# Optimization experiments

Hardware: AMD Instinct MI355X
Metric: run time of the kernel (lower is better)

The kernel has to match this reference:

```python
import jax, jax.numpy as jnp
import numpy as np

EPS = 1e-9       # module's displacement/convergence epsilon
COS_EPS = 1e-8   # torch F.cosine_similarity eps (norms clamped at eps)
LN_EPS = 1e-5


def _safe_norm(sq):
    # sqrt with zero-safe gradient for exactly-zero (padded) vectors
    return jnp.where(sq > 0, jnp.sqrt(jnp.maximum(sq, 1e-30)), 0.0)


def _features(coords, n):
    """coords: [S, md] padded; n: true length (>=4). Returns [60] features."""
    S, md = coords.shape
    f32 = coords.dtype
    nf = n.astype(f32)
    idx_d = jnp.arange(S - 1)
    m = n - 1                       # number of valid deltas
    mf = m.astype(f32)
    dmask = idx_d < m
    dmaskf = dmask.astype(f32)

    deltas = (coords[1:] - coords[:-1]) * dmaskf[:, None]     # [S-1, md]
    dmags = _safe_norm(jnp.sum(deltas * deltas, axis=-1))      # [S-1]

    last = jnp.take(coords, n - 1, axis=0)
    total_disp = _safe_norm(jnp.sum((last - coords[0]) ** 2))
    path_len = jnp.sum(dmags)
    disp_ratio = total_disp / (path_len + EPS)
    n_steps_norm = nf / 10.0

    # consecutive cosine similarities / curvatures (valid count = n-2)
    na = jnp.maximum(dmags, COS_EPS)
    cos = jnp.sum(deltas[:-1] * deltas[1:], axis=-1) / (na[:-1] * na[1:])  # [S-2]
    idx_c = jnp.arange(S - 2)
    cmask = idx_c < (n - 2)
    cmaskf = cmask.astype(f32)
    ncf = (n - 2).astype(f32)
    curv = 1.0 - cos
    curv_m = jnp.where(cmask, curv, 0.0)
    mean_curv = jnp.sum(curv_m) / ncf
    max_curv = jnp.max(jnp.where(cmask, curv, -jnp.inf))
    min_curv = jnp.min(jnp.where(cmask, curv, jnp.inf))
    curv_var = jnp.sum(cmaskf * (curv - mean_curv) ** 2) / jnp.maximum(ncf - 1.0, 1.0)
    std_curv = jnp.where(ncf > 1.0, jnp.sqrt(jnp.maximum(curv_var, 1e-30)), 0.0)
    curv_range = max_curv - min_curv

    mean_cos = jnp.sum(jnp.where(cmask, cos, 0.0)) / ncf
    min_cos = jnp.min(jnp.where(cmask, cos, jnp.inf))
    dir_changes = jnp.sum(cmaskf * (cos < 0).astype(f32)) / jnp.maximum(ncf, 1.0)

    linearity = disp_ratio
    loop_score = 1.0 - total_disp / (path_len + EPS)

    half = m // 2
    fmaskf = (idx_d < half + 1).astype(f32)
    smaskf = ((idx_d >= half) & (idx_d < m)).astype(f32)
    first_half = jnp.sum(dmags * fmaskf) / (half + 1).astype(f32)
    second_half = jnp.sum(dmags * smaskf) / (m - half).astype(f32)
    convergence = (first_half - second_half) / (first_half + EPS)
    cascade = (second_half - first_half) / (first_half + EPS)

    # all-pairs cosine (the O(n^2) block) via one GEMM per sample
    cosmat = (deltas @ deltas.T) / (na[:, None] * na[None, :])  # [S-1, S-1]
    pmask = (idx_d[:, None] < idx_d[None, :]) & (idx_d[None, :] < m)
    npairs = mf * (mf - 1.0) / 2.0
    parallelism = jnp.sum(jnp.where(pmask, cosmat, 0.0)) / jnp.maximum(npairs, 1.0)

    mean_dm = path_len / mf
    dm_var = jnp.sum(dmaskf * (dmags - mean_dm) ** 2) / jnp.maximum(mf - 1.0, 1.0)
    std_dm = jnp.where(mf > 1.0, jnp.sqrt(jnp.maximum(dm_var, 1e-30)), 0.0)
    max_dm = jnp.max(jnp.where(dmask, dmags, -jnp.inf))
    jump = jnp.where(mean_dm > EPS, max_dm / mean_dm, 1.0)

    rmaskf = (jnp.arange(S) < n).astype(f32)
    cnt = nf * md
    mean_coord = jnp.sum(coords * rmaskf[:, None]) / cnt
    coord_var = jnp.sum(rmaskf[:, None] * (coords - mean_coord) ** 2) / (cnt - 1.0)
    std_coord = jnp.sqrt(jnp.maximum(coord_var, 1e-30))

    scalars = jnp.stack([
        total_disp, path_len, disp_ratio, n_steps_norm,
        mean_curv, max_curv, std_curv, curv_range,
        mean_cos, min_cos, dir_changes,
        linearity, loop_score, convergence, parallelism, jump, cascade,
        mean_dm, std_dm, mean_coord, std_coord,
    ])  # [21]
    padded_deltas = deltas[:3].reshape(-1)   # [30] (masked -> already zero-padded)
    padded_curvs = curv_m[:9]                # [9]
    return jnp.concatenate([scalars, padded_deltas, padded_curvs])  # [60]


def setup_inputs() -> dict:
    key = jax.random.key(0)
    ks = jax.random.split(key, 4)
    B, S, md, H = 32768, 48, 10, 48
    coords = jax.random.normal(ks[0], (B, S, md), dtype=jnp.float32)
    lengths = jax.random.randint(ks[1], (B,), 4, S + 1, dtype=jnp.int32)
    W = jax.random.normal(ks[2], (60, H), dtype=jnp.float32) * 0.1
    b = jax.random.normal(ks[3], (H,), dtype=jnp.float32) * 0.01
    ln_w = jnp.ones((H,), dtype=jnp.float32)
    ln_b = jnp.zeros((H,), dtype=jnp.float32)
    return {"coords": coords, "lengths": lengths, "W": W, "b": b, "ln_w": ln_w, "ln_b": ln_b}


def reference(coords, lengths, W, b, ln_w, ln_b):
    feats = jax.vmap(_features)(coords, lengths)          # [B, 60]
    h = feats @ W + b                                     # [B, 48]
    mu = jnp.mean(h, axis=-1, keepdims=True)
    var = jnp.mean((h - mu) ** 2, axis=-1, keepdims=True)
    h = (h - mu) / jnp.sqrt(var + LN_EPS) * ln_w + ln_b
    return jax.nn.gelu(h, approximate=False)              # dropout is identity at eval
```

## Files before the change

### kernel.cpp

```cpp
#include <hip/hip_runtime.h>
#include <math.h>

static __device__ __forceinline__ float frcp(float x){ return __builtin_amdgcn_rcpf(x); }
static __device__ __forceinline__ float fsq (float x){ return __builtin_amdgcn_sqrtf(x); }

template<int CTRL>
static __device__ __forceinline__ float dppadd(float x){
  int t = __builtin_amdgcn_update_dpp(0, __float_as_int(x), CTRL, 0xf, 0xf, true);
  return x + __int_as_float(t);
}
template<int CTRL>
static __device__ __forceinline__ float dppmax(float x){
  int t = __builtin_amdgcn_update_dpp(__float_as_int(x), __float_as_int(x), CTRL, 0xf, 0xf, false);
  return fmaxf(x, __int_as_float(t));
}
template<int CTRL>
static __device__ __forceinline__ float dppmin(float x){
  int t = __builtin_amdgcn_update_dpp(__float_as_int(x), __float_as_int(x), CTRL, 0xf, 0xf, false);
  return fminf(x, __int_as_float(t));
}
static __device__ __forceinline__ float rsum16(float x){
  x = dppadd<0x111>(x); x = dppadd<0x112>(x);
  x = dppadd<0x114>(x); x = dppadd<0x118>(x);
  return __int_as_float(__builtin_amdgcn_ds_swizzle(__float_as_int(x), 0x1F0));
}
static __device__ __forceinline__ float rmax16(float x){
  x = dppmax<0x111>(x); x = dppmax<0x112>(x);
  x = dppmax<0x114>(x); x = dppmax<0x118>(x);
  return __int_as_float(__builtin_amdgcn_ds_swizzle(__float_as_int(x), 0x1F0));
}
static __device__ __forceinline__ float rmin16(float x){
  x = dppmin<0x111>(x); x = dppmin<0x112>(x);
  x = dppmin<0x114>(x); x = dppmin<0x118>(x);
  return __int_as_float(__builtin_amdgcn_ds_swizzle(__float_as_int(x), 0x1F0));
}
#define BC(P, x) __int_as_float(__builtin_amdgcn_ds_swizzle(__float_as_int(x), 0x10 | ((P) << 5)))

__global__ void transpose_w(const float* __restrict__ W, float* __restrict__ Wt){
  int idx = blockIdx.x * 256 + threadIdx.x;
  if (idx < 60 * 48) { int f = idx / 48, j = idx - f * 48; Wt[j * 60 + f] = W[idx]; }
}

template<bool USEWT>
__global__ __launch_bounds__(256)
void traj_kernel(const float* __restrict__ coords,
                 const int* __restrict__ lengths,
                 const float* __restrict__ Wsrc,
                 const float* __restrict__ bias,
                 const float* __restrict__ lnw,
                 const float* __restrict__ lnb,
                 float* __restrict__ out, int B)
{
  const int lane = threadIdx.x & 63;
  const int s    = lane & 15;
  const int grp  = (blockIdx.x * 4 + (threadIdx.x >> 6)) * 4 + (lane >> 4);
  const bool bvalid = (grp < B);
  const int b = bvalid ? grp : (B - 1);

  const int n = lengths[b];
  const int m = n - 1;
  const float* cp = coords + (size_t)b * 480;

  float c[3][10], cn[3][10];
#pragma unroll
  for (int q = 0; q < 3; ++q) {
    const float2* p = reinterpret_cast<const float2*>(cp + (q * 16 + s) * 10);
#pragma unroll
    for (int k = 0; k < 5; ++k) { float2 v = p[k]; c[q][2*k] = v.x; c[q][2*k+1] = v.y; }
  }
#pragma unroll
  for (int q = 0; q < 3; ++q) {
    const int row = q * 16 + s + 1;
    if (row < 48) {
      const float2* p = reinterpret_cast<const float2*>(cp + row * 10);
#pragma unroll
      for (int k = 0; k < 5; ++k) { float2 v = p[k]; cn[q][2*k] = v.x; cn[q][2*k+1] = v.y; }
    } else {
#pragma unroll
      for (int k = 0; k < 10; ++k) cn[q][k] = 0.f;
    }
  }

  float csl = 0.f, cs2l = 0.f;
#pragma unroll
  for (int q = 0; q < 3; ++q) {
    float t1 = 0.f, t2 = 0.f;
#pragma unroll
    for (int k = 0; k < 10; ++k) { t1 += c[q][k]; t2 = fmaf(c[q][k], c[q][k], t2); }
    const bool act = (q * 16 + s) < n;
    csl  += act ? t1 : 0.f;
    cs2l += act ? t2 : 0.f;
  }
  const float sum_c  = rsum16(csl);
  const float sum_c2 = rsum16(cs2l);

  float cc0[10];
#pragma unroll
  for (int k = 0; k < 10; ++k) cc0[k] = BC(0, c[0][k]);
  const int qs = (n - 1) >> 4, ssl = (n - 1) & 15;
  float tql = 0.f;
#pragma unroll
  for (int q = 0; q < 3; ++q) {
    float tq = 0.f;
#pragma unroll
    for (int k = 0; k < 10; ++k) { float t = c[q][k] - cc0[k]; tq = fmaf(t, t, tq); }
    tql = (s == ssl && q == qs) ? tq : tql;
  }
  const float tdq = rsum16(tql);
  const float total_disp = (tdq > 0.f) ? fsq(fmaxf(tdq, 1e-30f)) : 0.f;

  const int half = m >> 1;
  float d[3][10], inv[3];
  float path_l=0.f, dm2_l=0.f, maxdm_l=0.f, sf_l=0.f, ss_l=0.f, uu_l=0.f;
  float uk[10];
#pragma unroll
  for (int k = 0; k < 10; ++k) uk[k] = 0.f;
#pragma unroll
  for (int q = 0; q < 3; ++q) {
    const int j = q * 16 + s;
    float ds_ = 0.f;
#pragma unroll
    for (int k = 0; k < 10; ++k) { float dd = cn[q][k] - c[q][k]; d[q][k] = dd; ds_ = fmaf(dd, dd, ds_); }
    const float sn = (ds_ > 0.f) ? fsq(fmaxf(ds_, 1e-30f)) : 0.f;
    inv[q] = frcp(fmaxf(sn, 1e-8f));
    const bool jm = j < m;
    const float dm = jm ? sn : 0.f;
    path_l += dm;
    dm2_l  += jm ? ds_ : 0.f;
    maxdm_l = fmaxf(maxdm_l, dm);
    sf_l += (j <= half) ? dm : 0.f;
    ss_l += (j >= half) ? dm : 0.f;
    const float invm = jm ? inv[q] : 0.f;
#pragma unroll
    for (int k = 0; k < 10; ++k) uk[k] = fmaf(d[q][k], invm, uk[k]);
    uu_l = fmaf(ds_ * invm, invm, uu_l);
  }

  const int rotb = (((lane & 48) | ((lane + 1) & 15)) << 2);
  const float rinv0 = __int_as_float(__builtin_amdgcn_ds_bpermute(rotb, __float_as_int(inv[0])));
  const float rinv1 = __int_as_float(__builtin_amdgcn_ds_bpermute(rotb, __float_as_int(inv[1])));
  const float rinv2 = __int_as_float(__builtin_amdgcn_ds_bpermute(rotb, __float_as_int(inv[2])));
  float invn[3];
  invn[0] = (s < 15) ? rinv0 : rinv1;
  invn[1] = (s < 15) ? rinv1 : rinv2;
  invn[2] = (s < 15) ? rinv2 : 0.f;

  float cos_l=0.f, cos2_l=0.f, ng_l=0.f, maxc_l=-INFINITY, minc_l=INFINITY;
  float curv0 = 0.f;
#pragma unroll
  for (int q = 0; q < 3; ++q) {
    const int j = q * 16 + s;
    float dn[10];
    if (j + 2 < 48) {
      const float2* p = reinterpret_cast<const float2*>(cp + (j + 2) * 10);
#pragma unroll
      for (int k = 0; k < 5; ++k) { float2 v = p[k]; dn[2*k] = v.x - cn[q][2*k]; dn[2*k+1] = v.y - cn[q][2*k+1]; }
    } else {
#pragma unroll
      for (int k = 0; k < 10; ++k) dn[k] = 0.f;
    }
    float dot = 0.f;
#pragma unroll
    for (int k = 0; k < 10; ++k) dot = fmaf(d[q][k], dn[k], dot);
    const float cosv = dot * inv[q] * invn[q];
    const bool ca = j < (n - 2);
    const float cm = ca ? cosv : 0.f;
    cos_l += cm;
    cos2_l = fmaf(cm, cm, cos2_l);
    maxc_l = fmaxf(maxc_l, ca ? cosv : -INFINITY);
    minc_l = fminf(minc_l, ca ? cosv :  INFINITY);
    ng_l += (cm < 0.f) ? 1.f : 0.f;
    if (q == 0) curv0 = ca ? (1.f - cosv) : 0.f;
  }

  const float path_len = rsum16(path_l);
  const float sum_dm2  = rsum16(dm2_l);
  const float max_dm   = rmax16(maxdm_l);
  const float sum_f    = rsum16(sf_l);
  const float sum_s    = rsum16(ss_l);
  const float sum_cos  = rsum16(cos_l);
  const float sum_cos2 = rsum16(cos2_l);
  const float sum_ng   = rsum16(ng_l);
  const float max_cos  = rmax16(maxc_l);
  const float min_cos  = rmin16(minc_l);
  float Usq = 0.f;
#pragma unroll
  for (int k = 0; k < 10; ++k) { float Uk = rsum16(uk[k]); Usq = fmaf(Uk, Uk, Usq); }
  const float sum_uu = rsum16(uu_l);

  const float EPSf = 1e-9f;
  const float nf = (float)n, mf = (float)m, ncf = (float)(n - 2);
  const float rncf = frcp(ncf);
  const float disp_ratio = total_disp * frcp(path_len + EPSf);
  const float sum_cv  = ncf - sum_cos;
  const float mean_cv = sum_cv * rncf;
  const float sum_cv2 = fmaf(-2.f, sum_cos, ncf) + sum_cos2;
  const float cv_var  = (sum_cv2 - ncf * mean_cv * mean_cv) * frcp(fmaxf(ncf - 1.f, 1.f));
  const float std_cv  = fsq(fmaxf(cv_var, 1e-30f));
  const float max_cv  = 1.f - min_cos;
  const float cv_rng  = max_cos - min_cos;
  const float mean_cs = sum_cos * rncf;
  const float dirchg  = sum_ng * rncf;
  const float fh = sum_f * frcp((float)(half + 1));
  const float sh = sum_s * frcp((float)(m - half));
  const float conv = (fh - sh) * frcp(fh + EPSf);
  const float npairs = mf * (mf - 1.f) * 0.5f;
  const float par = (Usq - sum_uu) * 0.5f * frcp(npairs);
  const float mean_dm = path_len * frcp(mf);
  const float dm_var = (sum_dm2 - mf * mean_dm * mean_dm) * frcp(mf - 1.f);
  const float std_dm = fsq(fmaxf(dm_var, 1e-30f));
  const float jump = (mean_dm > EPSf) ? max_dm * frcp(mean_dm) : 1.f;
  const float cnt = nf * 10.f;
  const float mean_co = sum_c * frcp(cnt);
  const float co_var = (sum_c2 - cnt * mean_co * mean_co) * frcp(cnt - 1.f);
  const float std_co = fsq(fmaxf(co_var, 1e-30f));

  float feat[60];
  feat[0]  = total_disp;
  feat[1]  = path_len;
  feat[2]  = disp_ratio;
  feat[3]  = nf * 0.1f;
  feat[4]  = mean_cv;
  feat[5]  = max_cv;
  feat[6]  = std_cv;
  feat[7]  = cv_rng;
  feat[8]  = mean_cs;
  feat[9]  = min_cos;
  feat[10] = dirchg;
  feat[11] = disp_ratio;
  feat[12] = 1.f - disp_ratio;
  feat[13] = conv;
  feat[14] = par;
  feat[15] = jump;
  feat[16] = -conv;
  feat[17] = mean_dm;
  feat[18] = std_dm;
  feat[19] = mean_co;
  feat[20] = std_co;
#pragma unroll
  for (int k = 0; k < 10; ++k) feat[21 + k] = BC(0, d[0][k]);
#pragma unroll
  for (int k = 0; k < 10; ++k) feat[31 + k] = BC(1, d[0][k]);
#pragma unroll
  for (int k = 0; k < 10; ++k) feat[41 + k] = BC(2, d[0][k]);
  feat[51] = BC(0, curv0); feat[52] = BC(1, curv0); feat[53] = BC(2, curv0);
  feat[54] = BC(3, curv0); feat[55] = BC(4, curv0); feat[56] = BC(5, curv0);
  feat[57] = BC(6, curv0); feat[58] = BC(7, curv0); feat[59] = BC(8, curv0);

  float h[3];
#pragma unroll
  for (int q = 0; q < 3; ++q) {
    const int j = q * 16 + s;
    float acc = bias[j];
    if (USEWT) {
      const float4* wr = reinterpret_cast<const float4*>(Wsrc + j * 60);
#pragma unroll
      for (int t = 0; t < 15; ++t) {
        float4 w = wr[t];
        acc = fmaf(feat[4*t+0], w.x, acc);
        acc = fmaf(feat[4*t+1], w.y, acc);
        acc = fmaf(feat[4*t+2], w.z, acc);
        acc = fmaf(feat[4*t+3], w.w, acc);
      }
    } else {
#pragma unroll
      for (int f = 0; f < 60; ++f) acc = fmaf(feat[f], Wsrc[f * 48 + j], acc);
    }
    h[q] = acc;
  }

  const float s1 = rsum16(h[0] + h[1] + h[2]);
  const float s2 = rsum16(fmaf(h[0], h[0], fmaf(h[1], h[1], h[2] * h[2])));
  const float mu  = s1 * (1.f / 48.f);
  const float var = fmaf(-mu, mu, s2 * (1.f / 48.f));
  const float rstd = __builtin_amdgcn_rsqf(var + 1e-5f);

  if (bvalid) {
#pragma unroll
    for (int q = 0; q < 3; ++q) {
      const int j = q * 16 + s;
      float x = (h[q] - mu) * rstd * lnw[j] + lnb[j];
      float x2 = x * x;
      float u  = 0.7978845608f * x * fmaf(0.044715f, x2, 1.f);
      float e  = __builtin_amdgcn_exp2f(u * 2.885390082f);
      float th = fmaf(-2.f, frcp(1.f + e), 1.f);
      out[(size_t)b * 48 + j] = 0.5f * x * (1.f + th);
    }
  }
}

extern "C" void kernel_launch(void* const* d_in, const int* in_sizes, int n_in,
                              void* d_out, int out_size, void* d_ws, size_t ws_size,
                              hipStream_t stream)
{
  const float* coords = (const float*)d_in[0];
  const int*   lengths= (const int*)d_in[1];
  const float* W      = (const float*)d_in[2];
  const float* bias   = (const float*)d_in[3];
  const float* lnw    = (const float*)d_in[4];
  const float* lnb    = (const float*)d_in[5];
  float* out = (float*)d_out;

  const int B = in_sizes[1];
  const int blocks = (B + 15) / 16;

  if (ws_size >= (size_t)(60 * 48 * sizeof(float))) {
    float* Wt = (float*)d_ws;
    transpose_w<<<12, 256, 0, stream>>>(W, Wt);
    traj_kernel<true><<<blocks, 256, 0, stream>>>(coords, lengths, Wt, bias, lnw, lnb, out, B);
  } else {
    traj_kernel<false><<<blocks, 256, 0, stream>>>(coords, lengths, W, bias, lnw, lnb, out, B);
  }
}
```

Before: 122.3 us.

## Stage block's coordinates in LDS with coalesced float4 loads; split matvec accumulators

Each block of 16 trajectories now copies its whole contiguous coordinate slab (16x480 floats) into shared memory with coalesced float4 loads before any compute. All later strided row reads (current, next and next-next rows) come from LDS instead of global memory. This is meant to cut poorly coalesced, redundant global traffic, at the cost of 30KB of LDS per block, which may limit occupancy, plus a block barrier. Separately, the feature-by-weight dot product uses two independent accumulators to shorten the FMA dependency chain.

```diff
diff --git a/kernel.cpp b/kernel.cpp
--- a/kernel.cpp
+++ b/kernel.cpp
@@ -51,20 +51,39 @@
                  const float* __restrict__ lnb,
                  float* __restrict__ out, int B)
 {
-  const int lane = threadIdx.x & 63;
+  __shared__ float lds_c[16 * 480];
+
+  const int tid  = threadIdx.x;
+  const int lane = tid & 63;
   const int s    = lane & 15;
-  const int grp  = (blockIdx.x * 4 + (threadIdx.x >> 6)) * 4 + (lane >> 4);
+  const int T    = ((tid >> 6) << 2) | (lane >> 4);
+  const int blk  = blockIdx.x;
+  const int grp  = blk * 16 + T;
   const bool bvalid = (grp < B);
   const int b = bvalid ? grp : (B - 1);
 
+  {
+    const int lastblk = (B - 1) >> 4;
+    const int sblk = (blk <= lastblk) ? blk : lastblk;
+    const float4* g = reinterpret_cast<const float4*>(coords + (size_t)sblk * 7680);
+    float4* l = reinterpret_cast<float4*>(lds_c);
+    const int nvec = min(1920, (B - sblk * 16) * 120);
+#pragma unroll
+    for (int it = 0; it < 8; ++it) {
+      int idx = tid + it * 256;
+      if (idx < nvec) l[idx] = g[idx];
+    }
+  }
+  __syncthreads();
+
   const int n = lengths[b];
   const int m = n - 1;
-  const float* cp = coords + (size_t)b * 480;
+  const float* myc = lds_c + T * 480;
 
   float c[3][10], cn[3][10];
 #pragma unroll
   for (int q = 0; q < 3; ++q) {
-    const float2* p = reinterpret_cast<const float2*>(cp + (q * 16 + s) * 10);
+    const float2* p = reinterpret_cast<const float2*>(myc + (q * 16 + s) * 10);
 #pragma unroll
     for (int k = 0; k < 5; ++k) { float2 v = p[k]; c[q][2*k] = v.x; c[q][2*k+1] = v.y; }
   }
@@ -72,7 +91,7 @@
   for (int q = 0; q < 3; ++q) {
     const int row = q * 16 + s + 1;
     if (row < 48) {
-      const float2* p = reinterpret_cast<const float2*>(cp + row * 10);
+      const float2* p = reinterpret_cast<const float2*>(myc + row * 10);
 #pragma unroll
       for (int k = 0; k < 5; ++k) { float2 v = p[k]; cn[q][2*k] = v.x; cn[q][2*k+1] = v.y; }
     } else {
@@ -152,7 +171,7 @@
     const int j = q * 16 + s;
     float dn[10];
     if (j + 2 < 48) {
-      const float2* p = reinterpret_cast<const float2*>(cp + (j + 2) * 10);
+      const float2* p = reinterpret_cast<const float2*>(myc + (j + 2) * 10);
 #pragma unroll
       for (int k = 0; k < 5; ++k) { float2 v = p[k]; dn[2*k] = v.x - cn[q][2*k]; dn[2*k+1] = v.y - cn[q][2*k+1]; }
     } else {
@@ -251,22 +270,32 @@
 #pragma unroll
   for (int q = 0; q < 3; ++q) {
     const int j = q * 16 + s;
-    float acc = bias[j];
+    float acc0 = bias[j], acc1 = 0.f;
     if (USEWT) {
       const float4* wr = reinterpret_cast<const float4*>(Wsrc + j * 60);
 #pragma unroll
-      for (int t = 0; t < 15; ++t) {
+      for (int t = 0; t < 15; t += 2) {
         float4 w = wr[t];
-        acc = fmaf(feat[4*t+0], w.x, acc);
-        acc = fmaf(feat[4*t+1], w.y, acc);
-        acc = fmaf(feat[4*t+2], w.z, acc);
-        acc = fmaf(feat[4*t+3], w.w, acc);
+        acc0 = fmaf(feat[4*t+0], w.x, acc0);
+        acc0 = fmaf(feat[4*t+1], w.y, acc0);
+        acc0 = fmaf(feat[4*t+2], w.z, acc0);
+        acc0 = fmaf(feat[4*t+3], w.w, acc0);
+        if (t + 1 < 15) {
+          float4 w1 = wr[t+1];
+          acc1 = fmaf(feat[4*t+4], w1.x, acc1);
+          acc1 = fmaf(feat[4*t+5], w1.y, acc1);
+          acc1 = fmaf(feat[4*t+6], w1.z, acc1);
+          acc1 = fmaf(feat[4*t+7], w1.w, acc1);
+        }
       }
     } else {
 #pragma unroll
-      for (int f = 0; f < 60; ++f) acc = fmaf(feat[f], Wsrc[f * 48 + j], acc);
-    }
-    h[q] = acc;
+      for (int f = 0; f < 60; f += 2) {
+        acc0 = fmaf(feat[f],   Wsrc[f * 48 + j], acc0);
+        acc1 = fmaf(feat[f+1], Wsrc[(f+1) * 48 + j], acc1);
+      }
+    }
+    h[q] = acc0 + acc1;
   }
 
   const float s1 = rsum16(h[0] + h[1] + h[2]);
```

After: 125.6 us. +2.7%, slower.

## Stage W and features in LDS, reduce scalars in one lane

Applied to the files above, without the earlier changes.

The projection weights are now staged once per block in shared memory, and the 60 per-trajectory features are written to a per-group LDS buffer instead of being broadcast into every lane's registers. Reductions skip the final swizzle broadcast: lane 15, which holds the full 16-lane sum, computes all scalar features alone and stores them. Total displacement is computed directly from rows 0 and n-1 in that same lane. The aim is to cut register pressure (launch bounds now ask for 4 blocks per SM), swizzle traffic and redundant global W loads, at the cost of a block sync, LDS reads and serial scalar work in one lane.

```diff
diff --git a/kernel.cpp b/kernel.cpp
--- a/kernel.cpp
+++ b/kernel.cpp
@@ -19,30 +19,35 @@
   int t = __builtin_amdgcn_update_dpp(__float_as_int(x), __float_as_int(x), CTRL, 0xf, 0xf, false);
   return fminf(x, __int_as_float(t));
 }
-static __device__ __forceinline__ float rsum16(float x){
+static __device__ __forceinline__ float rsum16s(float x){
   x = dppadd<0x111>(x); x = dppadd<0x112>(x);
   x = dppadd<0x114>(x); x = dppadd<0x118>(x);
-  return __int_as_float(__builtin_amdgcn_ds_swizzle(__float_as_int(x), 0x1F0));
-}
-static __device__ __forceinline__ float rmax16(float x){
+  return x;
+}
+static __device__ __forceinline__ float rmax16s(float x){
   x = dppmax<0x111>(x); x = dppmax<0x112>(x);
   x = dppmax<0x114>(x); x = dppmax<0x118>(x);
-  return __int_as_float(__builtin_amdgcn_ds_swizzle(__float_as_int(x), 0x1F0));
-}
-static __device__ __forceinline__ float rmin16(float x){
+  return x;
+}
+static __device__ __forceinline__ float rmin16s(float x){
   x = dppmin<0x111>(x); x = dppmin<0x112>(x);
   x = dppmin<0x114>(x); x = dppmin<0x118>(x);
-  return __int_as_float(__builtin_amdgcn_ds_swizzle(__float_as_int(x), 0x1F0));
-}
-#define BC(P, x) __int_as_float(__builtin_amdgcn_ds_swizzle(__float_as_int(x), 0x10 | ((P) << 5)))
+  return x;
+}
+static __device__ __forceinline__ float rsum16b(float x){
+  return __int_as_float(__builtin_amdgcn_ds_swizzle(__float_as_int(rsum16s(x)), 0x1F0));
+}
 
 __global__ void transpose_w(const float* __restrict__ W, float* __restrict__ Wt){
   int idx = blockIdx.x * 256 + threadIdx.x;
   if (idx < 60 * 48) { int f = idx / 48, j = idx - f * 48; Wt[j * 60 + f] = W[idx]; }
 }
 
+#define WOFF 2880
+#define FSTR 72
+
 template<bool USEWT>
-__global__ __launch_bounds__(256)
+__global__ __launch_bounds__(256, 4)
 void traj_kernel(const float* __restrict__ coords,
                  const int* __restrict__ lengths,
                  const float* __restrict__ Wsrc,
@@ -51,15 +56,45 @@
                  const float* __restrict__ lnb,
                  float* __restrict__ out, int B)
 {
-  const int lane = threadIdx.x & 63;
+  __shared__ __align__(16) float lds[WOFF + 16 * FSTR];
+
+  const int tid  = threadIdx.x;
+  const int lane = tid & 63;
   const int s    = lane & 15;
-  const int grp  = (blockIdx.x * 4 + (threadIdx.x >> 6)) * 4 + (lane >> 4);
+  const int T    = ((tid >> 6) << 2) | (lane >> 4);
+  const int grp  = blockIdx.x * 16 + T;
   const bool bvalid = (grp < B);
   const int b = bvalid ? grp : (B - 1);
 
+  if (USEWT) {
+    for (int idx = tid; idx < 720; idx += 256)
+      reinterpret_cast<float4*>(lds)[idx] = reinterpret_cast<const float4*>(Wsrc)[idx];
+  } else {
+    for (int idx = tid; idx < 2880; idx += 256) {
+      int j = idx / 60, f = idx - j * 60;
+      lds[idx] = Wsrc[f * 48 + j];
+    }
+  }
+  __syncthreads();
+
   const int n = lengths[b];
   const int m = n - 1;
+  const int half = m >> 1;
   const float* cp = coords + (size_t)b * 480;
+
+  float total_disp = 0.f;
+  if (s == 15) {
+    const float2* p0 = reinterpret_cast<const float2*>(cp);
+    const float2* pl = reinterpret_cast<const float2*>(cp + (size_t)(n - 1) * 10);
+    float t = 0.f;
+#pragma unroll
+    for (int k = 0; k < 5; ++k) {
+      float2 a = p0[k], z = pl[k];
+      float dx = z.x - a.x, dy = z.y - a.y;
+      t = fmaf(dx, dx, fmaf(dy, dy, t));
+    }
+    total_disp = (t > 0.f) ? fsq(fmaxf(t, 1e-30f)) : 0.f;
+  }
 
   float c[3][10], cn[3][10];
 #pragma unroll
@@ -91,25 +126,7 @@
     csl  += act ? t1 : 0.f;
     cs2l += act ? t2 : 0.f;
   }
-  const float sum_c  = rsum16(csl);
-  const float sum_c2 = rsum16(cs2l);
-
-  float cc0[10];
-#pragma unroll
-  for (int k = 0; k < 10; ++k) cc0[k] = BC(0, c[0][k]);
-  const int qs = (n - 1) >> 4, ssl = (n - 1) & 15;
-  float tql = 0.f;
-#pragma unroll
-  for (int q = 0; q < 3; ++q) {
-    float tq = 0.f;
-#pragma unroll
-    for (int k = 0; k < 10; ++k) { float t = c[q][k] - cc0[k]; tq = fmaf(t, t, tq); }
-    tql = (s == ssl && q == qs) ? tq : tql;
-  }
-  const float tdq = rsum16(tql);
-  const float total_disp = (tdq > 0.f) ? fsq(fmaxf(tdq, 1e-30f)) : 0.f;
-
-  const int half = m >> 1;
+
   float d[3][10], inv[3];
   float path_l=0.f, dm2_l=0.f, maxdm_l=0.f, sf_l=0.f, ss_l=0.f, uu_l=0.f;
   float uk[10];
@@ -173,113 +190,105 @@
     if (q == 0) curv0 = ca ? (1.f - cosv) : 0.f;
   }
 
-  const float path_len = rsum16(path_l);
-  const float sum_dm2  = rsum16(dm2_l);
-  const float max_dm   = rmax16(maxdm_l);
-  const float sum_f    = rsum16(sf_l);
-  const float sum_s    = rsum16(ss_l);
-  const float sum_cos  = rsum16(cos_l);
-  const float sum_cos2 = rsum16(cos2_l);
-  const float sum_ng   = rsum16(ng_l);
-  const float max_cos  = rmax16(maxc_l);
-  const float min_cos  = rmin16(minc_l);
+  const float path_len = rsum16s(path_l);
+  const float sum_dm2  = rsum16s(dm2_l);
+  const float max_dm   = rmax16s(maxdm_l);
+  const float sum_f    = rsum16s(sf_l);
+  const float sum_s    = rsum16s(ss_l);
+  const float sum_cos  = rsum16s(cos_l);
+  const float sum_cos2 = rsum16s(cos2_l);
+  const float sum_ng   = rsum16s(ng_l);
+  const float max_cos  = rmax16s(maxc_l);
+  const float min_cos  = rmin16s(minc_l);
+  const float sum_c    = rsum16s(csl);
+  const float sum_c2   = rsum16s(cs2l);
   float Usq = 0.f;
 #pragma unroll
-  for (int k = 0; k < 10; ++k) { float Uk = rsum16(uk[k]); Usq = fmaf(Uk, Uk, Usq); }
-  const float sum_uu = rsum16(uu_l);
-
-  const float EPSf = 1e-9f;
-  const float nf = (float)n, mf = (float)m, ncf = (float)(n - 2);
-  const float rncf = frcp(ncf);
-  const float disp_ratio = total_disp * frcp(path_len + EPSf);
-  const float sum_cv  = ncf - sum_cos;
-  const float mean_cv = sum_cv * rncf;
-  const float sum_cv2 = fmaf(-2.f, sum_cos, ncf) + sum_cos2;
-  const float cv_var  = (sum_cv2 - ncf * mean_cv * mean_cv) * frcp(fmaxf(ncf - 1.f, 1.f));
-  const float std_cv  = fsq(fmaxf(cv_var, 1e-30f));
-  const float max_cv  = 1.f - min_cos;
-  const float cv_rng  = max_cos - min_cos;
-  const float mean_cs = sum_cos * rncf;
-  const float dirchg  = sum_ng * rncf;
-  const float fh = sum_f * frcp((float)(half + 1));
-  const float sh = sum_s * frcp((float)(m - half));
-  const float conv = (fh - sh) * frcp(fh + EPSf);
-  const float npairs = mf * (mf - 1.f) * 0.5f;
-  const float par = (Usq - sum_uu) * 0.5f * frcp(npairs);
-  const float mean_dm = path_len * frcp(mf);
-  const float dm_var = (sum_dm2 - mf * mean_dm * mean_dm) * frcp(mf - 1.f);
-  const float std_dm = fsq(fmaxf(dm_var, 1e-30f));
-  const float jump = (mean_dm > EPSf) ? max_dm * frcp(mean_dm) : 1.f;
-  const float cnt = nf * 10.f;
-  const float mean_co = sum_c * frcp(cnt);
-  const float co_var = (sum_c2 - cnt * mean_co * mean_co) * frcp(cnt - 1.f);
-  const float std_co = fsq(fmaxf(co_var, 1e-30f));
-
-  float feat[60];
-  feat[0]  = total_disp;
-  feat[1]  = path_len;
-  feat[2]  = disp_ratio;
-  feat[3]  = nf * 0.1f;
-  feat[4]  = mean_cv;
-  feat[5]  = max_cv;
-  feat[6]  = std_cv;
-  feat[7]  = cv_rng;
-  feat[8]  = mean_cs;
-  feat[9]  = min_cos;
-  feat[10] = dirchg;
-  feat[11] = disp_ratio;
-  feat[12] = 1.f - disp_ratio;
-  feat[13] = conv;
-  feat[14] = par;
-  feat[15] = jump;
-  feat[16] = -conv;
-  feat[17] = mean_dm;
-  feat[18] = std_dm;
-  feat[19] = mean_co;
-  feat[20] = std_co;
-#pragma unroll
-  for (int k = 0; k < 10; ++k) feat[21 + k] = BC(0, d[0][k]);
-#pragma unroll
-  for (int k = 0; k < 10; ++k) feat[31 + k] = BC(1, d[0][k]);
-#pragma unroll
-  for (int k = 0; k < 10; ++k) feat[41 + k] = BC(2, d[0][k]);
-  feat[51] = BC(0, curv0); feat[52] = BC(1, curv0); feat[53] = BC(2, curv0);
-  feat[54] = BC(3, curv0); feat[55] = BC(4, curv0); feat[56] = BC(5, curv0);
-  feat[57] = BC(6, curv0); feat[58] = BC(7, curv0); feat[59] = BC(8, curv0);
-
-  float h[3];
-#pragma unroll
-  for (int q = 0; q < 3; ++q) {
-    const int j = q * 16 + s;
-    float acc = bias[j];
-    if (USEWT) {
-      const float4* wr = reinterpret_cast<const float4*>(Wsrc + j * 60);
-#pragma unroll
-      for (int t = 0; t < 15; ++t) {
-        float4 w = wr[t];
-        acc = fmaf(feat[4*t+0], w.x, acc);
-        acc = fmaf(feat[4*t+1], w.y, acc);
-        acc = fmaf(feat[4*t+2], w.z, acc);
-        acc = fmaf(feat[4*t+3], w.w, acc);
-      }
-    } else {
-#pragma unroll
-      for (int f = 0; f < 60; ++f) acc = fmaf(feat[f], Wsrc[f * 48 + j], acc);
-    }
-    h[q] = acc;
-  }
-
-  const float s1 = rsum16(h[0] + h[1] + h[2]);
-  const float s2 = rsum16(fmaf(h[0], h[0], fmaf(h[1], h[1], h[2] * h[2])));
+  for (int k = 0; k < 10; ++k) { float Uk = rsum16s(uk[k]); Usq = fmaf(Uk, Uk, Usq); }
+  const float sum_uu = rsum16s(uu_l);
+
+  float* fb = lds + WOFF + T * FSTR;
+  if (s < 3) {
+#pragma unroll
+    for (int k = 0; k < 10; ++k) fb[21 + s * 10 + k] = d[0][k];
+  }
+  if (s < 9) fb[51 + s] = curv0;
+  if (s == 15) {
+    const float EPSf = 1e-9f;
+    const float nf = (float)n, mf = (float)m, ncf = (float)(n - 2);
+    const float rncf = frcp(ncf);
+    const float disp_ratio = total_disp * frcp(path_len + EPSf);
+    const float sum_cv  = ncf - sum_cos;
+    const float mean_cv = sum_cv * rncf;
+    const float sum_cv2 = fmaf(-2.f, sum_cos, ncf) + sum_cos2;
+    const float cv_var  = (sum_cv2 - ncf * mean_cv * mean_cv) * frcp(fmaxf(ncf - 1.f, 1.f));
+    const float std_cv  = fsq(fmaxf(cv_var, 1e-30f));
+    const float fh = sum_f * frcp((float)(half + 1));
+    const float sh = sum_s * frcp((float)(m - half));
+    const float conv = (fh - sh) * frcp(fh + EPSf);
+    const float npairs = mf * (mf - 1.f) * 0.5f;
+    const float par = (Usq - sum_uu) * 0.5f * frcp(npairs);
+    const float mean_dm = path_len * frcp(mf);
+    const float dm_var = (sum_dm2 - mf * mean_dm * mean_dm) * frcp(mf - 1.f);
+    const float std_dm = fsq(fmaxf(dm_var, 1e-30f));
+    const float jump = (mean_dm > EPSf) ? max_dm * frcp(mean_dm) : 1.f;
+    const float cnt = nf * 10.f;
+    const float mean_co = sum_c * frcp(cnt);
+    const float co_var = (sum_c2 - cnt * mean_co * mean_co) * frcp(cnt - 1.f);
+    const float std_co = fsq(fmaxf(co_var, 1e-30f));
+    fb[0]  = total_disp;
+    fb[1]  = path_len;
+    fb[2]  = disp_ratio;
+    fb[3]  = nf * 0.1f;
+    fb[4]  = mean_cv;
+    fb[5]  = 1.f - min_cos;
+    fb[6]  = std_cv;
+    fb[7]  = max_cos - min_cos;
+    fb[8]  = sum_cos * rncf;
+    fb[9]  = min_cos;
+    fb[10] = sum_ng * rncf;
+    fb[11] = disp_ratio;
+    fb[12] = 1.f - disp_ratio;
+    fb[13] = conv;
+    fb[14] = par;
+    fb[15] = jump;
+    fb[16] = -conv;
+    fb[17] = mean_dm;
+    fb[18] = std_dm;
+    fb[19] = mean_co;
+    fb[20] = std_co;
+  }
+  __builtin_amdgcn_wave_barrier();
+
+  float h0 = bias[s], h1 = bias[16 + s], h2 = bias[32 + s];
+  const float4* fbv = reinterpret_cast<const float4*>(fb);
+  const float4* w0  = reinterpret_cast<const float4*>(lds + (0 * 16 + s) * 60);
+  const float4* w1  = reinterpret_cast<const float4*>(lds + (1 * 16 + s) * 60);
+  const float4* w2  = reinterpret_cast<const float4*>(lds + (2 * 16 + s) * 60);
+#pragma unroll
+  for (int t = 0; t < 15; ++t) {
+    float4 fv = fbv[t];
+    float4 a = w0[t], bq = w1[t], cq = w2[t];
+    h0 = fmaf(fv.x, a.x, h0);  h0 = fmaf(fv.y, a.y, h0);
+    h0 = fmaf(fv.z, a.z, h0);  h0 = fmaf(fv.w, a.w, h0);
+    h1 = fmaf(fv.x, bq.x, h1); h1 = fmaf(fv.y, bq.y, h1);
+    h1 = fmaf(fv.z, bq.z, h1); h1 = fmaf(fv.w, bq.w, h1);
+    h2 = fmaf(fv.x, cq.x, h2); h2 = fmaf(fv.y, cq.y, h2);
+    h2 = fmaf(fv.z, cq.z, h2); h2 = fmaf(fv.w, cq.w, h2);
+  }
+
+  const float s1 = rsum16b(h0 + h1 + h2);
+  const float s2 = rsum16b(fmaf(h0, h0, fmaf(h1, h1, h2 * h2)));
   const float mu  = s1 * (1.f / 48.f);
   const float var = fmaf(-mu, mu, s2 * (1.f / 48.f));
   const float rstd = __builtin_amdgcn_rsqf(var + 1e-5f);
 
   if (bvalid) {
+    float hq[3] = {h0, h1, h2};
 #pragma unroll
     for (int q = 0; q < 3; ++q) {
       const int j = q * 16 + s;
-      float x = (h[q] - mu) * rstd * lnw[j] + lnb[j];
+      float x = (hq[q] - mu) * rstd * lnw[j] + lnb[j];
       float x2 = x * x;
       float u  = 0.7978845608f * x * fmaf(0.044715f, x2, 1.f);
       float e  = __builtin_amdgcn_exp2f(u * 2.885390082f);
```

Measured after the change: 139.6 us. 1.14x slower.

## Assign 32 lanes per trajectory instead of 16 to cut per-thread work

Applied to the files above, without the earlier changes.

Remaps the kernel so each trajectory is handled by a 32-lane half-wave with two row slots per lane, instead of a 16-lane group with three slots. Reductions and broadcasts move to 32-lane versions that use DPP plus two swizzles, and the block covers 8 trajectories instead of 16, so the grid doubles. The aim is lower register pressure and higher occupancy, plus shorter per-lane dependency chains. In exchange, total instruction count rises: half the lanes sit idle in the second slot, each reduction needs an extra swizzle and add, and the projection does more FMAs per trajectory overall.

```diff
diff --git a/kernel.cpp b/kernel.cpp
--- a/kernel.cpp
+++ b/kernel.cpp
@@ -19,22 +19,26 @@
   int t = __builtin_amdgcn_update_dpp(__float_as_int(x), __float_as_int(x), CTRL, 0xf, 0xf, false);
   return fminf(x, __int_as_float(t));
 }
-static __device__ __forceinline__ float rsum16(float x){
+template<int OFF>
+static __device__ __forceinline__ float swz(float x){
+  return __int_as_float(__builtin_amdgcn_ds_swizzle(__float_as_int(x), OFF));
+}
+static __device__ __forceinline__ float rsum32(float x){
   x = dppadd<0x111>(x); x = dppadd<0x112>(x);
   x = dppadd<0x114>(x); x = dppadd<0x118>(x);
-  return __int_as_float(__builtin_amdgcn_ds_swizzle(__float_as_int(x), 0x1F0));
-}
-static __device__ __forceinline__ float rmax16(float x){
+  return swz<0x1E0>(x) + swz<0x3E0>(x);
+}
+static __device__ __forceinline__ float rmax32(float x){
   x = dppmax<0x111>(x); x = dppmax<0x112>(x);
   x = dppmax<0x114>(x); x = dppmax<0x118>(x);
-  return __int_as_float(__builtin_amdgcn_ds_swizzle(__float_as_int(x), 0x1F0));
-}
-static __device__ __forceinline__ float rmin16(float x){
+  return fmaxf(swz<0x1E0>(x), swz<0x3E0>(x));
+}
+static __device__ __forceinline__ float rmin32(float x){
   x = dppmin<0x111>(x); x = dppmin<0x112>(x);
   x = dppmin<0x114>(x); x = dppmin<0x118>(x);
-  return __int_as_float(__builtin_amdgcn_ds_swizzle(__float_as_int(x), 0x1F0));
-}
-#define BC(P, x) __int_as_float(__builtin_amdgcn_ds_swizzle(__float_as_int(x), 0x10 | ((P) << 5)))
+  return fminf(swz<0x1E0>(x), swz<0x3E0>(x));
+}
+#define BC32(P, x) swz<((P) << 5)>(x)
 
 __global__ void transpose_w(const float* __restrict__ W, float* __restrict__ Wt){
   int idx = blockIdx.x * 256 + threadIdx.x;
@@ -51,142 +55,156 @@
                  const float* __restrict__ lnb,
                  float* __restrict__ out, int B)
 {
-  const int lane = threadIdx.x & 63;
-  const int s    = lane & 15;
-  const int grp  = (blockIdx.x * 4 + (threadIdx.x >> 6)) * 4 + (lane >> 4);
+  const int tid  = threadIdx.x;
+  const int lane = tid & 63;
+  const int w    = lane & 31;
+  const int T    = ((tid >> 6) << 1) | (lane >> 5);
+  const int grp  = blockIdx.x * 8 + T;
   const bool bvalid = (grp < B);
   const int b = bvalid ? grp : (B - 1);
 
   const int n = lengths[b];
   const int m = n - 1;
+  const int half = m >> 1;
   const float* cp = coords + (size_t)b * 480;
 
-  float c[3][10], cn[3][10];
-#pragma unroll
-  for (int q = 0; q < 3; ++q) {
-    const float2* p = reinterpret_cast<const float2*>(cp + (q * 16 + s) * 10);
-#pragma unroll
-    for (int k = 0; k < 5; ++k) { float2 v = p[k]; c[q][2*k] = v.x; c[q][2*k+1] = v.y; }
-  }
-#pragma unroll
-  for (int q = 0; q < 3; ++q) {
-    const int row = q * 16 + s + 1;
-    if (row < 48) {
-      const float2* p = reinterpret_cast<const float2*>(cp + row * 10);
-#pragma unroll
-      for (int k = 0; k < 5; ++k) { float2 v = p[k]; cn[q][2*k] = v.x; cn[q][2*k+1] = v.y; }
+  float c0[10], cn0[10], c1[10], cn1[10];
+  {
+    const float2* p = reinterpret_cast<const float2*>(cp + w * 10);
+#pragma unroll
+    for (int k = 0; k < 5; ++k){ float2 v = p[k]; c0[2*k]=v.x; c0[2*k+1]=v.y; }
+    p = reinterpret_cast<const float2*>(cp + (w + 1) * 10);
+#pragma unroll
+    for (int k = 0; k < 5; ++k){ float2 v = p[k]; cn0[2*k]=v.x; cn0[2*k+1]=v.y; }
+  }
+  if (w < 16) {
+    const float2* p = reinterpret_cast<const float2*>(cp + (32 + w) * 10);
+#pragma unroll
+    for (int k = 0; k < 5; ++k){ float2 v = p[k]; c1[2*k]=v.x; c1[2*k+1]=v.y; }
+    if (w < 15) {
+      p = reinterpret_cast<const float2*>(cp + (33 + w) * 10);
+#pragma unroll
+      for (int k = 0; k < 5; ++k){ float2 v = p[k]; cn1[2*k]=v.x; cn1[2*k+1]=v.y; }
     } else {
 #pragma unroll
-      for (int k = 0; k < 10; ++k) cn[q][k] = 0.f;
-    }
+      for (int k = 0; k < 10; ++k) cn1[k] = 0.f;
+    }
+  } else {
+#pragma unroll
+    for (int k = 0; k < 10; ++k) { c1[k] = 0.f; cn1[k] = 0.f; }
   }
 
   float csl = 0.f, cs2l = 0.f;
-#pragma unroll
-  for (int q = 0; q < 3; ++q) {
+  {
     float t1 = 0.f, t2 = 0.f;
 #pragma unroll
-    for (int k = 0; k < 10; ++k) { t1 += c[q][k]; t2 = fmaf(c[q][k], c[q][k], t2); }
-    const bool act = (q * 16 + s) < n;
-    csl  += act ? t1 : 0.f;
-    cs2l += act ? t2 : 0.f;
-  }
-  const float sum_c  = rsum16(csl);
-  const float sum_c2 = rsum16(cs2l);
-
-  float cc0[10];
-#pragma unroll
-  for (int k = 0; k < 10; ++k) cc0[k] = BC(0, c[0][k]);
-  const int qs = (n - 1) >> 4, ssl = (n - 1) & 15;
-  float tql = 0.f;
-#pragma unroll
-  for (int q = 0; q < 3; ++q) {
-    float tq = 0.f;
-#pragma unroll
-    for (int k = 0; k < 10; ++k) { float t = c[q][k] - cc0[k]; tq = fmaf(t, t, tq); }
-    tql = (s == ssl && q == qs) ? tq : tql;
-  }
-  const float tdq = rsum16(tql);
+    for (int k = 0; k < 10; ++k) { t1 += c0[k]; t2 = fmaf(c0[k], c0[k], t2); }
+    const bool a0 = w < n;
+    csl  += a0 ? t1 : 0.f;  cs2l += a0 ? t2 : 0.f;
+    t1 = 0.f; t2 = 0.f;
+#pragma unroll
+    for (int k = 0; k < 10; ++k) { t1 += c1[k]; t2 = fmaf(c1[k], c1[k], t2); }
+    const bool a1 = (w < 16) && (32 + w < n);
+    csl  += a1 ? t1 : 0.f;  cs2l += a1 ? t2 : 0.f;
+  }
+
+  float cc0k[10];
+#pragma unroll
+  for (int k = 0; k < 10; ++k) cc0k[k] = BC32(0, c0[k]);
+  const int ssl = (n - 1) & 31, qs = (n - 1) >> 5;
+  float tq0 = 0.f, tq1 = 0.f;
+#pragma unroll
+  for (int k = 0; k < 10; ++k) {
+    float t = c0[k] - cc0k[k]; tq0 = fmaf(t, t, tq0);
+    t = c1[k] - cc0k[k];       tq1 = fmaf(t, t, tq1);
+  }
+  const float tql = (w == ssl) ? (qs ? tq1 : tq0) : 0.f;
+  const float tdq = rsum32(tql);
   const float total_disp = (tdq > 0.f) ? fsq(fmaxf(tdq, 1e-30f)) : 0.f;
 
-  const int half = m >> 1;
-  float d[3][10], inv[3];
-  float path_l=0.f, dm2_l=0.f, maxdm_l=0.f, sf_l=0.f, ss_l=0.f, uu_l=0.f;
+  float d0[10], d1[10];
+  float ds0 = 0.f, ds1 = 0.f;
+#pragma unroll
+  for (int k = 0; k < 10; ++k) { float t = cn0[k] - c0[k]; d0[k] = t; ds0 = fmaf(t, t, ds0); }
+#pragma unroll
+  for (int k = 0; k < 10; ++k) { float t = cn1[k] - c1[k]; d1[k] = t; ds1 = fmaf(t, t, ds1); }
+  const float sn0 = (ds0 > 0.f) ? fsq(fmaxf(ds0, 1e-30f)) : 0.f;
+  const float sn1 = (ds1 > 0.f) ? fsq(fmaxf(ds1, 1e-30f)) : 0.f;
+  const float inv0 = frcp(fmaxf(sn0, 1e-8f));
+  const float inv1 = frcp(fmaxf(sn1, 1e-8f));
+  const bool dact0 = (w < m);
+  const bool dact1 = (w < 16) && (32 + w < m);
+  const float dm0 = dact0 ? sn0 : 0.f;
+  const float dm1 = dact1 ? sn1 : 0.f;
+  const float path_l  = dm0 + dm1;
+  const float dm2_l   = (dact0 ? ds0 : 0.f) + (dact1 ? ds1 : 0.f);
+  const float maxdm_l = fmaxf(dm0, dm1);
+  const float sf_l    = (w <= half) ? dm0 : 0.f;
+  const float ss_l    = ((w >= half) ? dm0 : 0.f) + dm1;
+  const float i0m = dact0 ? inv0 : 0.f, i1m = dact1 ? inv1 : 0.f;
   float uk[10];
 #pragma unroll
-  for (int k = 0; k < 10; ++k) uk[k] = 0.f;
-#pragma unroll
-  for (int q = 0; q < 3; ++q) {
-    const int j = q * 16 + s;
-    float ds_ = 0.f;
-#pragma unroll
-    for (int k = 0; k < 10; ++k) { float dd = cn[q][k] - c[q][k]; d[q][k] = dd; ds_ = fmaf(dd, dd, ds_); }
-    const float sn = (ds_ > 0.f) ? fsq(fmaxf(ds_, 1e-30f)) : 0.f;
-    inv[q] = frcp(fmaxf(sn, 1e-8f));
-    const bool jm = j < m;
-    const float dm = jm ? sn : 0.f;
-    path_l += dm;
-    dm2_l  += jm ? ds_ : 0.f;
-    maxdm_l = fmaxf(maxdm_l, dm);
-    sf_l += (j <= half) ? dm : 0.f;
-    ss_l += (j >= half) ? dm : 0.f;
-    const float invm = jm ? inv[q] : 0.f;
-#pragma unroll
-    for (int k = 0; k < 10; ++k) uk[k] = fmaf(d[q][k], invm, uk[k]);
-    uu_l = fmaf(ds_ * invm, invm, uu_l);
-  }
-
-  const int rotb = (((lane & 48) | ((lane + 1) & 15)) << 2);
-  const float rinv0 = __int_as_float(__builtin_amdgcn_ds_bpermute(rotb, __float_as_int(inv[0])));
-  const float rinv1 = __int_as_float(__builtin_amdgcn_ds_bpermute(rotb, __float_as_int(inv[1])));
-  const float rinv2 = __int_as_float(__builtin_amdgcn_ds_bpermute(rotb, __float_as_int(inv[2])));
-  float invn[3];
-  invn[0] = (s < 15) ? rinv0 : rinv1;
-  invn[1] = (s < 15) ? rinv1 : rinv2;
-  invn[2] = (s < 15) ? rinv2 : 0.f;
-
-  float cos_l=0.f, cos2_l=0.f, ng_l=0.f, maxc_l=-INFINITY, minc_l=INFINITY;
-  float curv0 = 0.f;
-#pragma unroll
-  for (int q = 0; q < 3; ++q) {
-    const int j = q * 16 + s;
-    float dn[10];
-    if (j + 2 < 48) {
-      const float2* p = reinterpret_cast<const float2*>(cp + (j + 2) * 10);
-#pragma unroll
-      for (int k = 0; k < 5; ++k) { float2 v = p[k]; dn[2*k] = v.x - cn[q][2*k]; dn[2*k+1] = v.y - cn[q][2*k+1]; }
-    } else {
-#pragma unroll
-      for (int k = 0; k < 10; ++k) dn[k] = 0.f;
-    }
-    float dot = 0.f;
-#pragma unroll
-    for (int k = 0; k < 10; ++k) dot = fmaf(d[q][k], dn[k], dot);
-    const float cosv = dot * inv[q] * invn[q];
-    const bool ca = j < (n - 2);
-    const float cm = ca ? cosv : 0.f;
-    cos_l += cm;
-    cos2_l = fmaf(cm, cm, cos2_l);
-    maxc_l = fmaxf(maxc_l, ca ? cosv : -INFINITY);
-    minc_l = fminf(minc_l, ca ? cosv :  INFINITY);
-    ng_l += (cm < 0.f) ? 1.f : 0.f;
-    if (q == 0) curv0 = ca ? (1.f - cosv) : 0.f;
-  }
-
-  const float path_len = rsum16(path_l);
-  const float sum_dm2  = rsum16(dm2_l);
-  const float max_dm   = rmax16(maxdm_l);
-  const float sum_f    = rsum16(sf_l);
-  const float sum_s    = rsum16(ss_l);
-  const float sum_cos  = rsum16(cos_l);
-  const float sum_cos2 = rsum16(cos2_l);
-  const float sum_ng   = rsum16(ng_l);
-  const float max_cos  = rmax16(maxc_l);
-  const float min_cos  = rmin16(minc_l);
+  for (int k = 0; k < 10; ++k) uk[k] = fmaf(d0[k], i0m, d1[k] * i1m);
+  const float uu_l = fmaf(ds0 * i0m, i0m, ds1 * i1m * i1m);
+
+  const int rotb = ((lane & 0x20) | ((w + 1) & 31)) << 2;
+  const float rinv0 = __int_as_float(__builtin_amdgcn_ds_bpermute(rotb, __float_as_int(inv0)));
+  const float rinv1 = __int_as_float(__builtin_amdgcn_ds_bpermute(rotb, __float_as_int(inv1)));
+  const float invn0 = (w < 31) ? rinv0 : rinv1;
+  const float invn1 = rinv1;
+
+  float cos_l, cos2_l, ng_l, maxc_l, minc_l, curv0;
+  {
+    float dot0 = 0.f;
+    {
+      const float2* p = reinterpret_cast<const float2*>(cp + (w + 2) * 10);
+#pragma unroll
+      for (int k = 0; k < 5; ++k) {
+        float2 v = p[k];
+        dot0 = fmaf(d0[2*k],   v.x - cn0[2*k],   dot0);
+        dot0 = fmaf(d0[2*k+1], v.y - cn0[2*k+1], dot0);
+      }
+    }
+    const float cosv0 = dot0 * inv0 * invn0;
+    const bool ca0 = w < (n - 2);
+    float dot1 = 0.f;
+    if (w < 14) {
+      const float2* p = reinterpret_cast<const float2*>(cp + (34 + w) * 10);
+#pragma unroll
+      for (int k = 0; k < 5; ++k) {
+        float2 v = p[k];
+        dot1 = fmaf(d1[2*k],   v.x - cn1[2*k],   dot1);
+        dot1 = fmaf(d1[2*k+1], v.y - cn1[2*k+1], dot1);
+      }
+    }
+    const float cosv1 = dot1 * inv1 * invn1;
+    const bool ca1 = (w < 16) && (32 + w < (n - 2));
+    const float cm0 = ca0 ? cosv0 : 0.f;
+    const float cm1 = ca1 ? cosv1 : 0.f;
+    cos_l  = cm0 + cm1;
+    cos2_l = fmaf(cm0, cm0, cm1 * cm1);
+    maxc_l = fmaxf(ca0 ? cosv0 : -INFINITY, ca1 ? cosv1 : -INFINITY);
+    minc_l = fminf(ca0 ? cosv0 :  INFINITY, ca1 ? cosv1 :  INFINITY);
+    ng_l   = ((cm0 < 0.f) ? 1.f : 0.f) + ((cm1 < 0.f) ? 1.f : 0.f);
+    curv0  = ca0 ? (1.f - cosv0) : 0.f;
+  }
+
+  const float path_len = rsum32(path_l);
+  const float sum_dm2  = rsum32(dm2_l);
+  const float max_dm   = rmax32(maxdm_l);
+  const float sum_f    = rsum32(sf_l);
+  const float sum_s    = rsum32(ss_l);
+  const float sum_cos  = rsum32(cos_l);
+  const float sum_cos2 = rsum32(cos2_l);
+  const float sum_ng   = rsum32(ng_l);
+  const float max_cos  = rmax32(maxc_l);
+  const float min_cos  = rmin32(minc_l);
+  const float sum_c    = rsum32(csl);
+  const float sum_c2   = rsum32(cs2l);
   float Usq = 0.f;
 #pragma unroll
-  for (int k = 0; k < 10; ++k) { float Uk = rsum16(uk[k]); Usq = fmaf(Uk, Uk, Usq); }
-  const float sum_uu = rsum16(uu_l);
+  for (int k = 0; k < 10; ++k) { float Uk = rsum32(uk[k]); Usq = fmaf(Uk, Uk, Usq); }
+  const float sum_uu = rsum32(uu_l);
 
   const float EPSf = 1e-9f;
   const float nf = (float)n, mf = (float)m, ncf = (float)(n - 2);
@@ -197,10 +215,6 @@
   const float sum_cv2 = fmaf(-2.f, sum_cos, ncf) + sum_cos2;
   const float cv_var  = (sum_cv2 - ncf * mean_cv * mean_cv) * frcp(fmaxf(ncf - 1.f, 1.f));
   const float std_cv  = fsq(fmaxf(cv_var, 1e-30f));
-  const float max_cv  = 1.f - min_cos;
-  const float cv_rng  = max_cos - min_cos;
-  const float mean_cs = sum_cos * rncf;
-  const float dirchg  = sum_ng * rncf;
   const float fh = sum_f * frcp((float)(half + 1));
   const float sh = sum_s * frcp((float)(m - half));
   const float conv = (fh - sh) * frcp(fh + EPSf);
@@ -221,12 +235,12 @@
   feat[2]  = disp_ratio;
   feat[3]  = nf * 0.1f;
   feat[4]  = mean_cv;
-  feat[5]  = max_cv;
+  feat[5]  = 1.f - min_cos;
   feat[6]  = std_cv;
-  feat[7]  = cv_rng;
-  feat[8]  = mean_cs;
+  feat[7]  = max_cos - min_cos;
+  feat[8]  = sum_cos * rncf;
   feat[9]  = min_cos;
-  feat[10] = dirchg;
+  feat[10] = sum_ng * rncf;
   feat[11] = disp_ratio;
   feat[12] = 1.f - disp_ratio;
   feat[13] = conv;
@@ -238,53 +252,59 @@
   feat[19] = mean_co;
   feat[20] = std_co;
 #pragma unroll
-  for (int k = 0; k < 10; ++k) feat[21 + k] = BC(0, d[0][k]);
-#pragma unroll
-  for (int k = 0; k < 10; ++k) feat[31 + k] = BC(1, d[0][k]);
-#pragma unroll
-  for (int k = 0; k < 10; ++k) feat[41 + k] = BC(2, d[0][k]);
-  feat[51] = BC(0, curv0); feat[52] = BC(1, curv0); feat[53] = BC(2, curv0);
-  feat[54] = BC(3, curv0); feat[55] = BC(4, curv0); feat[56] = BC(5, curv0);
-  feat[57] = BC(6, curv0); feat[58] = BC(7, curv0); feat[59] = BC(8, curv0);
-
-  float h[3];
-#pragma unroll
-  for (int q = 0; q < 3; ++q) {
-    const int j = q * 16 + s;
-    float acc = bias[j];
-    if (USEWT) {
-      const float4* wr = reinterpret_cast<const float4*>(Wsrc + j * 60);
-#pragma unroll
-      for (int t = 0; t < 15; ++t) {
-        float4 w = wr[t];
-        acc = fmaf(feat[4*t+0], w.x, acc);
-        acc = fmaf(feat[4*t+1], w.y, acc);
-        acc = fmaf(feat[4*t+2], w.z, acc);
-        acc = fmaf(feat[4*t+3], w.w, acc);
-      }
-    } else {
-#pragma unroll
-      for (int f = 0; f < 60; ++f) acc = fmaf(feat[f], Wsrc[f * 48 + j], acc);
-    }
-    h[q] = acc;
-  }
-
-  const float s1 = rsum16(h[0] + h[1] + h[2]);
-  const float s2 = rsum16(fmaf(h[0], h[0], fmaf(h[1], h[1], h[2] * h[2])));
+  for (int k = 0; k < 10; ++k) feat[21 + k] = BC32(0, d0[k]);
+#pragma unroll
+  for (int k = 0; k < 10; ++k) feat[31 + k] = BC32(1, d0[k]);
+#pragma unroll
+  for (int k = 0; k < 10; ++k) feat[41 + k] = BC32(2, d0[k]);
+  feat[51] = BC32(0, curv0); feat[52] = BC32(1, curv0); feat[53] = BC32(2, curv0);
+  feat[54] = BC32(3, curv0); feat[55] = BC32(4, curv0); feat[56] = BC32(5, curv0);
+  feat[57] = BC32(6, curv0); feat[58] = BC32(7, curv0); feat[59] = BC32(8, curv0);
+
+  const int j1 = 32 + (w & 15);
+  float h0 = bias[w], h1 = bias[j1];
+  if (USEWT) {
+    const float4* w0 = reinterpret_cast<const float4*>(Wsrc + w  * 60);
+    const float4* w1 = reinterpret_cast<const float4*>(Wsrc + j1 * 60);
+#pragma unroll
+    for (int t = 0; t < 15; ++t) {
+      float4 a = w0[t], bq = w1[t];
+      h0 = fmaf(feat[4*t+0], a.x, h0);  h0 = fmaf(feat[4*t+1], a.y, h0);
+      h0 = fmaf(feat[4*t+2], a.z, h0);  h0 = fmaf(feat[4*t+3], a.w, h0);
+      h1 = fmaf(feat[4*t+0], bq.x, h1); h1 = fmaf(feat[4*t+1], bq.y, h1);
+      h1 = fmaf(feat[4*t+2], bq.z, h1); h1 = fmaf(feat[4*t+3], bq.w, h1);
+    }
+  } else {
+#pragma unroll
+    for (int f = 0; f < 60; ++f) {
+      h0 = fmaf(feat[f], Wsrc[f * 48 + w],  h0);
+      h1 = fmaf(feat[f], Wsrc[f * 48 + j1], h1);
+    }
+  }
+
+  const float h1m = (w < 16) ? h1 : 0.f;
+  const float s1 = rsum32(h0 + h1m);
+  const float s2 = rsum32(fmaf(h0, h0, h1m * h1m));
   const float mu  = s1 * (1.f / 48.f);
   const float var = fmaf(-mu, mu, s2 * (1.f / 48.f));
   const float rstd = __builtin_amdgcn_rsqf(var + 1e-5f);
 
   if (bvalid) {
-#pragma unroll
-    for (int q = 0; q < 3; ++q) {
-      const int j = q * 16 + s;
-      float x = (h[q] - mu) * rstd * lnw[j] + lnb[j];
+    {
+      float x = (h0 - mu) * rstd * lnw[w] + lnb[w];
       float x2 = x * x;
       float u  = 0.7978845608f * x * fmaf(0.044715f, x2, 1.f);
       float e  = __builtin_amdgcn_exp2f(u * 2.885390082f);
       float th = fmaf(-2.f, frcp(1.f + e), 1.f);
-      out[(size_t)b * 48 + j] = 0.5f * x * (1.f + th);
+      out[(size_t)b * 48 + w] = 0.5f * x * (1.f + th);
+    }
+    if (w < 16) {
+      float x = (h1 - mu) * rstd * lnw[j1] + lnb[j1];
+      float x2 = x * x;
+      float u  = 0.7978845608f * x * fmaf(0.044715f, x2, 1.f);
+      float e  = __builtin_amdgcn_exp2f(u * 2.885390082f);
+      float th = fmaf(-2.f, frcp(1.f + e), 1.f);
+      out[(size_t)b * 48 + j1] = 0.5f * x * (1.f + th);
     }
   }
 }
@@ -302,7 +322,7 @@
   float* out = (float*)d_out;
 
   const int B = in_sizes[1];
-  const int blocks = (B + 15) / 16;
+  const int blocks = (B + 7) / 8;
 
   if (ws_size >= (size_t)(60 * 48 * sizeof(float))) {
     float* Wt = (float*)d_ws;
```

New measurement: 131.6 us. 7.6% more time.
